# Kernel optimization log

Measured on AMD Instinct MI355X. Metric: run time of the kernel, lower is better.

## Reference

```python
import jax, jax.numpy as jnp
import numpy as np

N = 50000
E = 800000
EPS = 1e-16
NEG_SLOPE = 0.2

def setup_inputs() -> dict:
    key = jax.random.key(0)
    ks = jax.random.split(key, 10)
    s = lambda fan: 1.0 / np.sqrt(fan)
    return {
        "x": jax.random.normal(ks[0], (N, 128), dtype=jnp.float32),
        "edge_index": jax.random.randint(ks[1], (2, E), 0, N, dtype=jnp.int64),
        "W1": jax.random.normal(ks[2], (128, 4 * 32), dtype=jnp.float32) * s(128),
        "att_src1": jax.random.normal(ks[3], (4, 32), dtype=jnp.float32) * s(32),
        "att_dst1": jax.random.normal(ks[4], (4, 32), dtype=jnp.float32) * s(32),
        "b1": jnp.zeros((128,), dtype=jnp.float32),
        "W2": jax.random.normal(ks[5], (128, 2), dtype=jnp.float32) * s(128),
        "att_src2": jax.random.normal(ks[6], (1, 2), dtype=jnp.float32) * s(2),
        "att_dst2": jax.random.normal(ks[7], (1, 2), dtype=jnp.float32) * s(2),
        "b2": jnp.zeros((2,), dtype=jnp.float32),
    }

def _gat_conv(x, src, dst, W, att_src, att_dst, bias, heads, out_ch, concat):
    n = x.shape[0]
    h = (x @ W).reshape(n, heads, out_ch)                      # [N,H,C]
    a_src = jnp.sum(h * att_src[None], axis=-1)                # [N,H]
    a_dst = jnp.sum(h * att_dst[None], axis=-1)                # [N,H]
    e = jax.nn.leaky_relu(a_src[src] + a_dst[dst], NEG_SLOPE)  # [Etot,H]
    # segment softmax over incoming edges per destination node
    m = jax.ops.segment_max(e, dst, num_segments=n)            # [N,H]
    m = jnp.where(jnp.isfinite(m), m, 0.0)
    ex = jnp.exp(e - m[dst])
    denom = jax.ops.segment_sum(ex, dst, num_segments=n)       # [N,H]
    alpha = ex / (denom[dst] + EPS)                            # [Etot,H]
    out = jax.ops.segment_sum(alpha[:, :, None] * h[src], dst, num_segments=n)  # [N,H,C]
    if concat:
        out = out.reshape(n, heads * out_ch)
    else:
        out = out.mean(axis=1)
    return out + bias

def reference(x, edge_index, W1, att_src1, att_dst1, b1, W2, att_src2, att_dst2, b2):
    n = x.shape[0]
    # PyG GATConv adds self-loops by default
    loops = jnp.arange(n, dtype=edge_index.dtype)
    src = jnp.concatenate([edge_index[0], loops])
    dst = jnp.concatenate([edge_index[1], loops])
    # dropout is identity at inference
    h = jax.nn.elu(_gat_conv(x, src, dst, W1, att_src1, att_dst1, b1, 4, 32, True))
    h = _gat_conv(h, src, dst, W2, att_src2, att_dst2, b2, 1, 2, False)
    return jax.nn.log_softmax(h, axis=1)
```

## Files before the change

### kernel.cpp

```cpp
#include <hip/hip_runtime.h>
#include <hip/hip_bf16.h>

#define NN 50000
#define EE 800000
#define CAP 64
#define CSTRIDE 16
#define NEG_SLOPE 0.2f
#define EPSF 1e-16f
#define BUILD_BLOCKS 4096
#define GEMM_BLOCKS ((NN + 63) / 64)
#define NPAIRS (EE / 2)

typedef unsigned int uint32;
typedef __attribute__((ext_vector_type(8))) short short8;
typedef __attribute__((ext_vector_type(4))) float floatx4;

__device__ __forceinline__ unsigned short f2bf(float f) {
  unsigned int u = __float_as_uint(f);
  unsigned int r = (u + 0x7fffu + ((u >> 16) & 1u)) >> 16;
  return (unsigned short)r;
}
__device__ __forceinline__ float bf_lo(uint32 v) { return __uint_as_float(v << 16); }
__device__ __forceinline__ float bf_hi(uint32 v) { return __uint_as_float(v & 0xffff0000u); }

__global__ __launch_bounds__(256) void prep_zero_k(
    const float* __restrict__ W1, unsigned short* __restrict__ Wt,
    int* __restrict__ counts) {
  const int step = gridDim.x * 256;
  const int t0 = blockIdx.x * 256 + threadIdx.x;
  for (int i = t0; i < NN * CSTRIDE; i += step)
    counts[i] = ((i & (CSTRIDE - 1)) == 0) ? 1 : 0;
  for (int i = t0; i < 128 * 128; i += step) {
    int k = i >> 7, c = i & 127;
    Wt[c * 128 + k] = f2bf(W1[i]);
  }
}

__global__ __launch_bounds__(256) void build_k(
    const int* __restrict__ ei, int* __restrict__ counts,
    int* __restrict__ csr) {
  const int b = blockIdx.x;
  const int range = b & 7;
  const int lo = range * (NN / 8);
  const int hi = lo + (NN / 8);
  const int group = b >> 3;
  const int tid0 = group * 256 + threadIdx.x;
  const int stride = (BUILD_BLOCKS >> 3) * 256;

  {
    int n = lo + tid0;
    if (n < hi) csr[n * CAP] = n;
  }

  const int2* __restrict__ dst2 = (const int2*)(ei + EE);
  const int2* __restrict__ src2 = (const int2*)(ei);
  for (int p = tid0; p < NPAIRS; p += stride) {
    int2 d2 = dst2[p];
    int2 s2 = src2[p];
    if (d2.x >= lo && d2.x < hi) {
      int r = atomicAdd(&counts[d2.x * CSTRIDE], 1);
      if (r < CAP) csr[d2.x * CAP + r] = s2.x;
    }
    if (d2.y >= lo && d2.y < hi) {
      int r = atomicAdd(&counts[d2.y * CSTRIDE], 1);
      if (r < CAP) csr[d2.y * CAP + r] = s2.y;
    }
  }
}

__global__ __launch_bounds__(256) void gemm_k(
    const float* __restrict__ x, const unsigned short* __restrict__ Wt,
    const float* __restrict__ att_src1, const float* __restrict__ att_dst1,
    uint32* __restrict__ h1b, float* __restrict__ as1, float* __restrict__ ad1) {
  const int tile = blockIdx.x;
  const int t    = threadIdx.x;
  const int wave = t >> 6;
  const int lane = t & 63;
  const int quad = lane >> 4;
  const int col  = lane & 15;
  const int nodeBase = tile * 64 + wave * 16;

  floatx4 acc[8];
  #pragma unroll
  for (int i = 0; i < 8; i++) acc[i] = (floatx4){0.f, 0.f, 0.f, 0.f};

  int mread = nodeBase + col; if (mread >= NN) mread = NN - 1;
  const float* __restrict__ xrow = x + (size_t)mread * 128 + quad * 8;
  const unsigned short* __restrict__ bbase = Wt + col * 128 + quad * 8;

  #pragma unroll
  for (int ks = 0; ks < 4; ks++) {
    float4 a0 = *(const float4*)(xrow + ks * 32);
    float4 a1 = *(const float4*)(xrow + ks * 32 + 4);
    union { short8 v; unsigned short u[8]; } af;
    af.u[0] = f2bf(a0.x); af.u[1] = f2bf(a0.y);
    af.u[2] = f2bf(a0.z); af.u[3] = f2bf(a0.w);
    af.u[4] = f2bf(a1.x); af.u[5] = f2bf(a1.y);
    af.u[6] = f2bf(a1.z); af.u[7] = f2bf(a1.w);
    #pragma unroll
    for (int tt = 0; tt < 8; tt++) {
      short8 bf = *(const short8*)(bbase + tt * 16 * 128 + ks * 32);
      acc[tt] = __builtin_amdgcn_mfma_f32_16x16x32_bf16(af.v, bf, acc[tt], 0, 0, 0);
    }
  }

  float asv[8], adv[8];
  #pragma unroll
  for (int tt = 0; tt < 8; tt++) {
    asv[tt] = att_src1[tt * 16 + col];
    adv[tt] = att_dst1[tt * 16 + col];
  }

  #pragma unroll
  for (int r = 0; r < 4; r++) {
    const int gn = nodeBase + quad * 4 + r;
    const bool live = (gn < NN);
    #pragma unroll
    for (int tt = 0; tt < 8; tt++) {
      float v = acc[tt][r];
      float w = __shfl_xor(v, 1, 64);
      if (live && ((col & 1) == 0)) {
        uint32 pk = (uint32)f2bf(v) | ((uint32)f2bf(w) << 16);
        h1b[(size_t)gn * 64 + tt * 8 + (col >> 1)] = pk;
      }
    }
    #pragma unroll
    for (int h = 0; h < 4; h++) {
      float ps = acc[2 * h][r] * asv[2 * h] + acc[2 * h + 1][r] * asv[2 * h + 1];
      float pd = acc[2 * h][r] * adv[2 * h] + acc[2 * h + 1][r] * adv[2 * h + 1];
      #pragma unroll
      for (int off = 1; off < 16; off <<= 1) {
        ps += __shfl_xor(ps, off, 64);
        pd += __shfl_xor(pd, off, 64);
      }
      if (live && col == 0) {
        as1[gn * 4 + h] = ps;
        ad1[gn * 4 + h] = pd;
      }
    }
  }
}

__global__ __launch_bounds__(256) void agg1_k(
    const int* __restrict__ counts, const int* __restrict__ csr,
    const uint32* __restrict__ h1b, const float* __restrict__ as1,
    const float* __restrict__ ad1, const float* __restrict__ b1,
    const float* __restrict__ W2, const float* __restrict__ att_src2,
    const float* __restrict__ att_dst2, float4* __restrict__ rec) {
  const int lane = threadIdx.x & 63;
  const int wv = threadIdx.x >> 6;
  const int hd = lane >> 4;
  const int n = __builtin_amdgcn_readfirstlane(blockIdx.x * 4 + wv);

  int cnt = counts[n * CSTRIDE];
  cnt = __builtin_amdgcn_readfirstlane(cnt < CAP ? cnt : CAP);
  const int* __restrict__ row = csr + n * CAP;
  const float adv = ad1[n * 4 + hd];

  float den = 0.f, accx = 0.f, accy = 0.f;
  int j = 0;
  for (; j + 3 < cnt; j += 4) {
    int s0 = row[j], s1 = row[j + 1], s2 = row[j + 2], s3 = row[j + 3];
    float e0 = as1[s0 * 4 + hd] + adv;
    float e1 = as1[s1 * 4 + hd] + adv;
    float e2 = as1[s2 * 4 + hd] + adv;
    float e3 = as1[s3 * 4 + hd] + adv;
    uint32 v0 = h1b[s0 * 64 + lane];
    uint32 v1 = h1b[s1 * 64 + lane];
    uint32 v2 = h1b[s2 * 64 + lane];
    uint32 v3 = h1b[s3 * 64 + lane];
    e0 = (e0 > 0.f) ? e0 : NEG_SLOPE * e0;
    e1 = (e1 > 0.f) ? e1 : NEG_SLOPE * e1;
    e2 = (e2 > 0.f) ? e2 : NEG_SLOPE * e2;
    e3 = (e3 > 0.f) ? e3 : NEG_SLOPE * e3;
    float x0 = __expf(e0), x1 = __expf(e1), x2 = __expf(e2), x3 = __expf(e3);
    den += (x0 + x1) + (x2 + x3);
    accx = fmaf(x0, bf_lo(v0), accx);
    accy = fmaf(x0, bf_hi(v0), accy);
    accx = fmaf(x1, bf_lo(v1), accx);
    accy = fmaf(x1, bf_hi(v1), accy);
    accx = fmaf(x2, bf_lo(v2), accx);
    accy = fmaf(x2, bf_hi(v2), accy);
    accx = fmaf(x3, bf_lo(v3), accx);
    accy = fmaf(x3, bf_hi(v3), accy);
  }
  for (; j < cnt; j++) {
    int s = row[j];
    float e = as1[s * 4 + hd] + adv;
    e = (e > 0.f) ? e : NEG_SLOPE * e;
    float ex = __expf(e);
    uint32 v = h1b[s * 64 + lane];
    den += ex;
    accx = fmaf(ex, bf_lo(v), accx);
    accy = fmaf(ex, bf_hi(v), accy);
  }

  float inv = 1.f / (den + EPSF);
  float2 bb = ((const float2*)b1)[lane];
  float ox = accx * inv + bb.x;
  float oy = accy * inv + bb.y;
  ox = (ox > 0.f) ? ox : (__expf(ox) - 1.f);
  oy = (oy > 0.f) ? oy : (__expf(oy) - 1.f);

  float4 wq = ((const float4*)W2)[lane];
  float p0 = ox * wq.x + oy * wq.z;
  float p1 = ox * wq.y + oy * wq.w;
  #pragma unroll
  for (int off = 32; off; off >>= 1) {
    p0 += __shfl_xor(p0, off, 64);
    p1 += __shfl_xor(p1, off, 64);
  }
  if (lane == 0) {
    rec[n] = make_float4(p0, p1,
                         p0 * att_src2[0] + p1 * att_src2[1],
                         p0 * att_dst2[0] + p1 * att_dst2[1]);
  }
}

__global__ __launch_bounds__(256) void agg2_k(
    const int* __restrict__ counts, const int* __restrict__ csr,
    const float4* __restrict__ rec, const float* __restrict__ b2,
    float* __restrict__ out) {
  int i = blockIdx.x * 256 + threadIdx.x;
  if (i >= NN * 8) return;
  int n = i >> 3;
  int sub = i & 7;
  const float adv = rec[n].w;
  int cnt = counts[n * CSTRIDE];
  cnt = cnt < CAP ? cnt : CAP;
  const int* __restrict__ row = csr + n * CAP;

  float den = 0.f, a0 = 0.f, a1 = 0.f;
  for (int j = sub; j < cnt; j += 8) {
    int s = row[j];
    float4 rs = rec[s];
    float e = rs.z + adv;
    e = (e > 0.f) ? e : NEG_SLOPE * e;
    float ex = __expf(e);
    den += ex;
    a0 = fmaf(ex, rs.x, a0);
    a1 = fmaf(ex, rs.y, a1);
  }
  #pragma unroll
  for (int off = 4; off; off >>= 1) {
    den += __shfl_down(den, off, 8);
    a0  += __shfl_down(a0, off, 8);
    a1  += __shfl_down(a1, off, 8);
  }
  if (sub == 0) {
    float inv = 1.f / (den + EPSF);
    float o0 = a0 * inv + b2[0];
    float o1 = a1 * inv + b2[1];
    float mx = fmaxf(o0, o1);
    float lse = mx + __logf(__expf(o0 - mx) + __expf(o1 - mx));
    *(float2*)&out[n * 2] = make_float2(o0 - lse, o1 - lse);
  }
}

extern "C" void kernel_launch(void* const* d_in, const int* in_sizes, int n_in,
                              void* d_out, int out_size, void* d_ws, size_t ws_size,
                              hipStream_t stream) {
  const float* x        = (const float*)d_in[0];
  const int*   ei       = (const int*)d_in[1];
  const float* W1       = (const float*)d_in[2];
  const float* att_src1 = (const float*)d_in[3];
  const float* att_dst1 = (const float*)d_in[4];
  const float* b1       = (const float*)d_in[5];
  const float* W2       = (const float*)d_in[6];
  const float* att_src2 = (const float*)d_in[7];
  const float* att_dst2 = (const float*)d_in[8];
  const float* b2       = (const float*)d_in[9];
  float* out = (float*)d_out;

  char* p = (char*)d_ws;
  auto alloc = [&](size_t bytes) {
    char* r = p;
    p += (bytes + 255) & ~size_t(255);
    return r;
  };
  uint32* h1b  = (uint32*)alloc(sizeof(uint32) * NN * 64);
  float* as1   = (float*)alloc(sizeof(float) * NN * 4);
  float* ad1   = (float*)alloc(sizeof(float) * NN * 4);
  float4* rec  = (float4*)alloc(sizeof(float4) * NN);
  int*   counts = (int*)alloc(sizeof(int) * NN * CSTRIDE);
  int*   csr   = (int*)alloc(sizeof(int) * NN * CAP);
  unsigned short* Wt = (unsigned short*)alloc(sizeof(unsigned short) * 128 * 128);

  prep_zero_k<<<512, 256, 0, stream>>>(W1, Wt, counts);
  build_k<<<BUILD_BLOCKS, 256, 0, stream>>>(ei, counts, csr);
  gemm_k<<<GEMM_BLOCKS, 256, 0, stream>>>(x, Wt, att_src1, att_dst1,
                                          h1b, as1, ad1);
  agg1_k<<<NN / 4, 256, 0, stream>>>(counts, csr, h1b, as1, ad1, b1, W2,
                                     att_src2, att_dst2, rec);
  agg2_k<<<(NN * 8 + 255) / 256, 256, 0, stream>>>(counts, csr, rec, b2, out);
}
```

Measured before the change: 192.5 us.

## Merge CSR build and GEMM into one launch; scalarize neighbor indices in agg1

The CSR build and the layer-1 GEMM are independent, so they now run as one kernel that dispatches by block index. This lets the atomic-heavy build work overlap with the MFMA GEMM tiles and saves one launch. In agg1 the neighbor indices are read with readfirstlane so they live in scalar registers and the address math is uniform across the wave. Leaky ReLU becomes a fmaxf. The merged kernel's register and occupancy needs are set by the heavier GEMM path, which may lower occupancy for the build blocks.

```diff
diff --git a/kernel.cpp b/kernel.cpp
--- a/kernel.cpp
+++ b/kernel.cpp
@@ -22,6 +22,7 @@
 }
 __device__ __forceinline__ float bf_lo(uint32 v) { return __uint_as_float(v << 16); }
 __device__ __forceinline__ float bf_hi(uint32 v) { return __uint_as_float(v & 0xffff0000u); }
+__device__ __forceinline__ float lrelu(float e) { return fmaxf(e, NEG_SLOPE * e); }
 
 __global__ __launch_bounds__(256) void prep_zero_k(
     const float* __restrict__ W1, unsigned short* __restrict__ Wt,
@@ -36,10 +37,9 @@
   }
 }
 
-__global__ __launch_bounds__(256) void build_k(
-    const int* __restrict__ ei, int* __restrict__ counts,
-    int* __restrict__ csr) {
-  const int b = blockIdx.x;
+__device__ __forceinline__ void do_build(int b, const int* __restrict__ ei,
+                                         int* __restrict__ counts,
+                                         int* __restrict__ csr) {
   const int range = b & 7;
   const int lo = range * (NN / 8);
   const int hi = lo + (NN / 8);
@@ -47,10 +47,7 @@
   const int tid0 = group * 256 + threadIdx.x;
   const int stride = (BUILD_BLOCKS >> 3) * 256;
 
-  {
-    int n = lo + tid0;
-    if (n < hi) csr[n * CAP] = n;
-  }
+  { int n = lo + tid0; if (n < hi) csr[n * CAP] = n; }
 
   const int2* __restrict__ dst2 = (const int2*)(ei + EE);
   const int2* __restrict__ src2 = (const int2*)(ei);
@@ -68,11 +65,10 @@
   }
 }
 
-__global__ __launch_bounds__(256) void gemm_k(
-    const float* __restrict__ x, const unsigned short* __restrict__ Wt,
+__device__ __forceinline__ void do_gemm_tile(
+    int tile, const float* __restrict__ x, const unsigned short* __restrict__ Wt,
     const float* __restrict__ att_src1, const float* __restrict__ att_dst1,
     uint32* __restrict__ h1b, float* __restrict__ as1, float* __restrict__ ad1) {
-  const int tile = blockIdx.x;
   const int t    = threadIdx.x;
   const int wave = t >> 6;
   const int lane = t & 63;
@@ -141,6 +137,19 @@
   }
 }
 
+__global__ __launch_bounds__(256) void work_k(
+    const int* __restrict__ ei, int* __restrict__ counts, int* __restrict__ csr,
+    const float* __restrict__ x, const unsigned short* __restrict__ Wt,
+    const float* __restrict__ att_src1, const float* __restrict__ att_dst1,
+    uint32* __restrict__ h1b, float* __restrict__ as1, float* __restrict__ ad1) {
+  const int b = blockIdx.x;
+  if (b < BUILD_BLOCKS) {
+    do_build(b, ei, counts, csr);
+  } else {
+    do_gemm_tile(b - BUILD_BLOCKS, x, Wt, att_src1, att_dst1, h1b, as1, ad1);
+  }
+}
+
 __global__ __launch_bounds__(256) void agg1_k(
     const int* __restrict__ counts, const int* __restrict__ csr,
     const uint32* __restrict__ h1b, const float* __restrict__ as1,
@@ -160,7 +169,10 @@
   float den = 0.f, accx = 0.f, accy = 0.f;
   int j = 0;
   for (; j + 3 < cnt; j += 4) {
-    int s0 = row[j], s1 = row[j + 1], s2 = row[j + 2], s3 = row[j + 3];
+    int s0 = __builtin_amdgcn_readfirstlane(row[j]);
+    int s1 = __builtin_amdgcn_readfirstlane(row[j + 1]);
+    int s2 = __builtin_amdgcn_readfirstlane(row[j + 2]);
+    int s3 = __builtin_amdgcn_readfirstlane(row[j + 3]);
     float e0 = as1[s0 * 4 + hd] + adv;
     float e1 = as1[s1 * 4 + hd] + adv;
     float e2 = as1[s2 * 4 + hd] + adv;
@@ -169,10 +181,7 @@
     uint32 v1 = h1b[s1 * 64 + lane];
     uint32 v2 = h1b[s2 * 64 + lane];
     uint32 v3 = h1b[s3 * 64 + lane];
-    e0 = (e0 > 0.f) ? e0 : NEG_SLOPE * e0;
-    e1 = (e1 > 0.f) ? e1 : NEG_SLOPE * e1;
-    e2 = (e2 > 0.f) ? e2 : NEG_SLOPE * e2;
-    e3 = (e3 > 0.f) ? e3 : NEG_SLOPE * e3;
+    e0 = lrelu(e0); e1 = lrelu(e1); e2 = lrelu(e2); e3 = lrelu(e3);
     float x0 = __expf(e0), x1 = __expf(e1), x2 = __expf(e2), x3 = __expf(e3);
     den += (x0 + x1) + (x2 + x3);
     accx = fmaf(x0, bf_lo(v0), accx);
@@ -185,9 +194,8 @@
     accy = fmaf(x3, bf_hi(v3), accy);
   }
   for (; j < cnt; j++) {
-    int s = row[j];
-    float e = as1[s * 4 + hd] + adv;
-    e = (e > 0.f) ? e : NEG_SLOPE * e;
+    int s = __builtin_amdgcn_readfirstlane(row[j]);
+    float e = lrelu(as1[s * 4 + hd] + adv);
     float ex = __expf(e);
     uint32 v = h1b[s * 64 + lane];
     den += ex;
@@ -234,8 +242,7 @@
   for (int j = sub; j < cnt; j += 8) {
     int s = row[j];
     float4 rs = rec[s];
-    float e = rs.z + adv;
-    e = (e > 0.f) ? e : NEG_SLOPE * e;
+    float e = lrelu(rs.z + adv);
     float ex = __expf(e);
     den += ex;
     a0 = fmaf(ex, rs.x, a0);
@@ -287,9 +294,8 @@
   unsigned short* Wt = (unsigned short*)alloc(sizeof(unsigned short) * 128 * 128);
 
   prep_zero_k<<<512, 256, 0, stream>>>(W1, Wt, counts);
-  build_k<<<BUILD_BLOCKS, 256, 0, stream>>>(ei, counts, csr);
-  gemm_k<<<GEMM_BLOCKS, 256, 0, stream>>>(x, Wt, att_src1, att_dst1,
-                                          h1b, as1, ad1);
+  work_k<<<BUILD_BLOCKS + GEMM_BLOCKS, 256, 0, stream>>>(
+      ei, counts, csr, x, Wt, att_src1, att_dst1, h1b, as1, ad1);
   agg1_k<<<NN / 4, 256, 0, stream>>>(counts, csr, h1b, as1, ad1, b1, W2,
                                      att_src2, att_dst2, rec);
   agg2_k<<<(NN * 8 + 255) / 256, 256, 0, stream>>>(counts, csr, rec, b2, out);
```

Measured after the change: 188.9 us. No clear change (-1.8%).
